# Kernel optimization log

Hardware: AMD Instinct MI355X
Metric: run time of the kernel (lower is better)

Reference implementation:

```python
import jax, jax.numpy as jnp
import numpy as np

EPS = 1e-6
HEADS = 8


def _block_weights(gh, gw):
    # block centers at (i+0.5, j+0.5); 'cos' transform, column-normalized (sum over dim 0)
    ii, jj = np.meshgrid(np.arange(gh) + 0.5, np.arange(gw) + 0.5, indexing='ij')
    centers = np.stack([ii.ravel(), jj.ravel()], axis=-1)  # [N, 2]
    d = np.linalg.norm(centers[:, None, :] - centers[None, :, :], axis=-1)  # [N, N]
    mat = np.cos(d / d.max() * np.pi / 4.0)
    mat = mat / mat.sum(axis=0, keepdims=True)
    return jnp.asarray(mat, dtype=jnp.float32)


def setup_inputs() -> dict:
    key = jax.random.key(0)
    ks = jax.random.split(key, 5)
    B, N, W, C = 8, 256, 49, 512
    s = 1.0 / np.sqrt(C)
    return {
        'x': jax.random.normal(ks[0], (B, N, W, C), jnp.float32),
        'ln_g': jnp.ones((C,), jnp.float32),
        'ln_b': jnp.zeros((C,), jnp.float32),
        'w_qkv': jax.random.normal(ks[1], (3 * C, C), jnp.float32) * s,  # Linear(dim, 3*dim, bias=False)
        'lepe_w': jax.random.normal(ks[2], (C, 1, 5, 5), jnp.float32) * 0.2,  # depthwise 5x5
        'lepe_b': jnp.zeros((C,), jnp.float32),
        'w_out': jax.random.normal(ks[3], (C, C), jnp.float32) * s,
        'b_out': jnp.zeros((C,), jnp.float32),
    }


def reference(x, ln_g, ln_b, w_qkv, lepe_w, lepe_b, w_out, b_out):
    B, N, Wn, C = x.shape
    H = HEADS
    D = C // H
    gh = gw = int(round(N ** 0.5))   # grid of window blocks
    wh = ww = int(round(Wn ** 0.5))  # tokens per window side

    # LayerNorm over channel dim (torch eps=1e-5, biased var)
    mu = x.mean(-1, keepdims=True)
    var = x.var(-1, keepdims=True)
    xn = (x - mu) / jnp.sqrt(var + 1e-5) * ln_g + ln_b

    # qkv projection
    qkv = jnp.einsum('bnwc,oc->bnwo', xn, w_qkv)
    q, k, v = jnp.split(qkv, 3, axis=-1)  # each [B, N, W, C]

    # LePE: fold v to image [B, C, gh*wh, gw*ww], depthwise conv 5x5 pad 2, unfold back
    img = v.reshape(B, gh, gw, wh, ww, C).transpose(0, 5, 1, 3, 2, 4).reshape(B, C, gh * wh, gw * ww)
    lepe = jax.lax.conv_general_dilated(
        img, lepe_w, window_strides=(1, 1), padding=((2, 2), (2, 2)),
        dimension_numbers=('NCHW', 'OIHW', 'NCHW'), feature_group_count=C)
    lepe = lepe + lepe_b[None, :, None, None]
    lepe = lepe.reshape(B, C, gh, wh, gw, ww).transpose(0, 2, 4, 3, 5, 1).reshape(B, N, Wn, C)

    # ReLU + eps feature maps (qk_norm=False -> identity norms)
    q = jax.nn.relu(q) + EPS
    k = jax.nn.relu(k) + EPS

    # split heads: [B, H, N, W, D]
    def split_heads(t):
        return t.reshape(B, N, Wn, H, D).transpose(0, 3, 1, 2, 4)
    q, k, v = split_heads(q), split_heads(k), split_heads(v)

    # per-block k^T v state: [B, H, N, D, D]
    kv = jnp.einsum('bhnwd,bhnwe->bhnde', k, v)
    weight = _block_weights(gh, gw)  # [N, N]
    kv = jnp.einsum('ij,bhjde->bhide', weight, kv)

    k_sum = k.sum(axis=-2)  # [B, H, N, D]
    qk_sum = jnp.einsum('bhnwd,bhnd->bhnw', q, k_sum)[..., None]  # [B, H, N, W, 1]
    normalizer = jnp.einsum('ij,bhjwo->bhiwo', weight, qk_sum) + EPS

    out = jnp.einsum('bhnwd,bhnde->bhnwe', q, kv) / normalizer  # [B, H, N, W, D]
    out = out.transpose(0, 2, 3, 1, 4).reshape(B, N, Wn, C)
    out = out + lepe
    return jnp.einsum('bnwc,oc->bnwo', out, w_out) + b_out
```

## Files before the change

### kernel.cpp

```cpp
#include <hip/hip_runtime.h>
#include <cstdint>

typedef unsigned short u16;
typedef unsigned int   u32;
typedef u16   u16x8 __attribute__((ext_vector_type(8)));
typedef u16   u16x4 __attribute__((ext_vector_type(4)));
typedef float f32x4 __attribute__((ext_vector_type(4)));
typedef __bf16 bf16x8 __attribute__((ext_vector_type(8)));

#define NB    256
#define WTOK  49
#define CH    512
#define HEADS 8
#define DH    64
#define TOK   100352
#define CO    1536

__device__ __forceinline__ u16 f2bf(float f) {
  u32 u = __float_as_uint(f);
  u = (u + 0x7FFFu + ((u >> 16) & 1u)) >> 16;
  return (u16)u;
}
__device__ __forceinline__ float bf2f(u16 u) { return __uint_as_float(((u32)u) << 16); }

__device__ __forceinline__ void load_lds16(const void* g, void* l) {
  __builtin_amdgcn_global_load_lds(
      reinterpret_cast<__attribute__((address_space(1))) void*>(reinterpret_cast<uintptr_t>(g)),
      reinterpret_cast<__attribute__((address_space(3))) void*>(reinterpret_cast<uintptr_t>(l)),
      16, 0, 0);
}

__global__ void cvt_f32_bf16(const float* __restrict__ in, u16* __restrict__ out, int n8) {
  int i = blockIdx.x * 256 + threadIdx.x;
  if (i < n8) {
    f32x4 a = *(const f32x4*)(in + (long)i * 8);
    f32x4 b = *(const f32x4*)(in + (long)i * 8 + 4);
    u16x8 o;
    o[0]=f2bf(a[0]); o[1]=f2bf(a[1]); o[2]=f2bf(a[2]); o[3]=f2bf(a[3]);
    o[4]=f2bf(b[0]); o[5]=f2bf(b[1]); o[6]=f2bf(b[2]); o[7]=f2bf(b[3]);
    *(u16x8*)(out + (long)i * 8) = o;
  }
}

__global__ void prep_wle(const float* __restrict__ lepe_w, float* __restrict__ wle) {
  int i = blockIdx.x * 256 + threadIdx.x;
  if (i < 12800) {
    int c = i / 25, kk = i % 25;
    wle[kk * 512 + c] = lepe_w[i];
  }
}

__global__ void weight_kernel(u16* __restrict__ Wbf, float* __restrict__ Wt) {
  int j = blockIdx.x, i = threadIdx.x;
  float iy = (float)(i >> 4) + 0.5f, ix = (float)(i & 15) + 0.5f;
  float jy = (float)(j >> 4) + 0.5f, jx = (float)(j & 15) + 0.5f;
  float dy = iy - jy, dx = ix - jx;
  float d = sqrtf(dy * dy + dx * dx);
  const float dmax = 21.213203435596427f;
  float m = cosf(d * (0.78539816339744831f / dmax));
  __shared__ float red[256];
  red[i] = m;
  __syncthreads();
  for (int s = 128; s > 0; s >>= 1) {
    if (i < s) red[i] += red[i + s];
    __syncthreads();
  }
  float w = m / red[0];
  Wbf[i * 256 + j] = f2bf(w);
  Wt[j * 256 + i] = w;
}

__global__ __launch_bounds__(256) void ln_kernel(const float* __restrict__ x,
                                                 const float* __restrict__ g,
                                                 const float* __restrict__ bta,
                                                 u16* __restrict__ xn) {
  int wave = threadIdx.x >> 6, lane = threadIdx.x & 63;
  long t = (long)blockIdx.x * 4 + wave;
  const float* xp = x + t * CH + lane * 8;
  f32x4 a = *(const f32x4*)xp;
  f32x4 b = *(const f32x4*)(xp + 4);
  float s  = a[0]+a[1]+a[2]+a[3]+b[0]+b[1]+b[2]+b[3];
  float sq = a[0]*a[0]+a[1]*a[1]+a[2]*a[2]+a[3]*a[3]+b[0]*b[0]+b[1]*b[1]+b[2]*b[2]+b[3]*b[3];
  for (int m = 1; m < 64; m <<= 1) { s += __shfl_xor(s, m); sq += __shfl_xor(sq, m); }
  float mu = s * (1.0f / 512.0f);
  float var = sq * (1.0f / 512.0f) - mu * mu;
  float rstd = rsqrtf(var + 1e-5f);
  const float* gp = g + lane * 8;
  const float* bp = bta + lane * 8;
  f32x4 g0 = *(const f32x4*)gp, g1 = *(const f32x4*)(gp + 4);
  f32x4 b0 = *(const f32x4*)bp, b1 = *(const f32x4*)(bp + 4);
  u16x8 o;
  o[0] = f2bf((a[0]-mu)*rstd*g0[0] + b0[0]);
  o[1] = f2bf((a[1]-mu)*rstd*g0[1] + b0[1]);
  o[2] = f2bf((a[2]-mu)*rstd*g0[2] + b0[2]);
  o[3] = f2bf((a[3]-mu)*rstd*g0[3] + b0[3]);
  o[4] = f2bf((b[0]-mu)*rstd*g1[0] + b1[0]);
  o[5] = f2bf((b[1]-mu)*rstd*g1[1] + b1[1]);
  o[6] = f2bf((b[2]-mu)*rstd*g1[2] + b1[2]);
  o[7] = f2bf((b[3]-mu)*rstd*g1[3] + b1[3]);
  *(u16x8*)(xn + t * CH + lane * 8) = o;
}

template <int KT>
__device__ __forceinline__ void kstep9(char* sm, const u16* sA, const u16* sB,
                                       int t, int lane_off, int wm, int wn,
                                       f32x4 (&acc)[8][4], bf16x8 (&fa)[2][8], bf16x8 (&fb)[2][4]) {
  constexpr int cur = KT & 1, nxt = cur ^ 1;
  if constexpr (KT + 4 < 16) {
    char* wbp = sm + ((KT + 4) & 3) * 32768 + t * 16;
    load_lds16(sA + (KT + 4) * 32, wbp);
    load_lds16(sA + (KT + 4) * 32 + 65536, wbp + 8192);
    load_lds16(sB + (KT + 4) * 32, wbp + 16384);
    load_lds16(sB + (KT + 4) * 32 + 65536, wbp + 24576);
  }
  if constexpr (KT + 1 < 16) {
    const char* base = sm + ((KT + 1) & 3) * 32768 + lane_off;
#pragma unroll
    for (int n = 0; n < 4; n++) fb[nxt][n] = *(const bf16x8*)(base + 16384 + wn * 4096 + n * 1024);
#pragma unroll
    for (int m = 0; m < 8; m++) fa[nxt][m] = *(const bf16x8*)(base + wm * 8192 + m * 1024);
  }
  __builtin_amdgcn_s_setprio(1);
#pragma unroll
  for (int m = 0; m < 8; m++)
#pragma unroll
    for (int n = 0; n < 4; n++)
      acc[m][n] = __builtin_amdgcn_mfma_f32_16x16x32_bf16(fa[cur][m], fb[cur][n], acc[m][n], 0, 0, 0);
  __builtin_amdgcn_s_setprio(0);
  if constexpr (KT < 14) {
    asm volatile("s_waitcnt lgkmcnt(0)" ::: "memory");
  }
  if constexpr (KT + 4 < 16) {
    asm volatile("s_waitcnt vmcnt(8)" ::: "memory");
  } else if constexpr (KT == 12) {
    asm volatile("s_waitcnt vmcnt(4)" ::: "memory");
  } else if constexpr (KT == 13) {
    asm volatile("s_waitcnt vmcnt(0)" ::: "memory");
  }
  if constexpr (KT < 14) __builtin_amdgcn_s_barrier();
}

template <int EPI>
__global__ __launch_bounds__(512, 2)
void gemm8(const u16* __restrict__ A, const u16* __restrict__ B,
           void* __restrict__ C, const float* __restrict__ bias, int N, int nbn) {
  __shared__ __align__(16) char sm[131072];
  const int nwg = gridDim.x;
  const int bid = blockIdx.x;
  const int cpx = nwg >> 3;
  const int vid = (bid & 7) * cpx + (bid >> 3);
  const int bn = vid % nbn, bm = vid / nbn;
  const int t = threadIdx.x;
  const int lane = t & 63, wave = t >> 6;
  const int wm = wave >> 2, wn = wave & 3;
  const int fr = lane & 15, fq = lane >> 4;
  const int lane_off = (fr >> 1) * 128 + ((((fr & 1) << 2) + fq) ^ (fr >> 1)) * 16;
  const int sl = (t & 7) ^ ((t >> 3) & 7);
  const u16* sA = A + ((long)bm * 256 + ((t >> 3) << 1) + (sl >> 2)) * 512 + (sl & 3) * 8;
  const u16* sB = B + ((long)bn * 256 + ((t >> 3) << 1) + (sl >> 2)) * 512 + (sl & 3) * 8;
  f32x4 acc[8][4] = {};
  bf16x8 fa[2][8], fb[2][4];
#pragma unroll
  for (int kt = 0; kt < 4; kt++) {
    char* d = sm + kt * 32768 + t * 16;
    load_lds16(sA + kt * 32, d);
    load_lds16(sA + kt * 32 + 65536, d + 8192);
    load_lds16(sB + kt * 32, d + 16384);
    load_lds16(sB + kt * 32 + 65536, d + 24576);
  }
  asm volatile("s_waitcnt vmcnt(8)" ::: "memory");
  __builtin_amdgcn_s_barrier();
  {
    const char* base = sm + lane_off;
#pragma unroll
    for (int n = 0; n < 4; n++) fb[0][n] = *(const bf16x8*)(base + 16384 + wn * 4096 + n * 1024);
#pragma unroll
    for (int m = 0; m < 8; m++) fa[0][m] = *(const bf16x8*)(base + wm * 8192 + m * 1024);
  }
  asm volatile("s_waitcnt lgkmcnt(0)" ::: "memory");
  __builtin_amdgcn_s_barrier();
  kstep9<0>(sm, sA, sB, t, lane_off, wm, wn, acc, fa, fb);
  kstep9<1>(sm, sA, sB, t, lane_off, wm, wn, acc, fa, fb);
  kstep9<2>(sm, sA, sB, t, lane_off, wm, wn, acc, fa, fb);
  kstep9<3>(sm, sA, sB, t, lane_off, wm, wn, acc, fa, fb);
  kstep9<4>(sm, sA, sB, t, lane_off, wm, wn, acc, fa, fb);
  kstep9<5>(sm, sA, sB, t, lane_off, wm, wn, acc, fa, fb);
  kstep9<6>(sm, sA, sB, t, lane_off, wm, wn, acc, fa, fb);
  kstep9<7>(sm, sA, sB, t, lane_off, wm, wn, acc, fa, fb);
  kstep9<8>(sm, sA, sB, t, lane_off, wm, wn, acc, fa, fb);
  kstep9<9>(sm, sA, sB, t, lane_off, wm, wn, acc, fa, fb);
  kstep9<10>(sm, sA, sB, t, lane_off, wm, wn, acc, fa, fb);
  kstep9<11>(sm, sA, sB, t, lane_off, wm, wn, acc, fa, fb);
  kstep9<12>(sm, sA, sB, t, lane_off, wm, wn, acc, fa, fb);
  kstep9<13>(sm, sA, sB, t, lane_off, wm, wn, acc, fa, fb);
  kstep9<14>(sm, sA, sB, t, lane_off, wm, wn, acc, fa, fb);
  kstep9<15>(sm, sA, sB, t, lane_off, wm, wn, acc, fa, fb);
  const long r0 = (long)bm * 256 + wm * 128 + fq * 4;
  const int c0 = bn * 256 + wn * 64 + fr;
#pragma unroll
  for (int m = 0; m < 8; m++) {
#pragma unroll
    for (int n = 0; n < 4; n++) {
      int c = c0 + n * 16;
#pragma unroll
      for (int jj = 0; jj < 4; jj++) {
        long r = r0 + m * 16 + jj;
        float v = acc[m][n][jj];
        if (EPI == 1) {
          if (c < 1024) v = fmaxf(v, 0.0f) + 1e-6f;
          ((u16*)C)[r * N + c] = f2bf(v);
        } else if (EPI == 2) {
          ((float*)C)[r * N + c] = v + bias[c];
        } else {
          ((u16*)C)[r * N + c] = f2bf(v);
        }
      }
    }
  }
}

template <int EPI>
__global__ __launch_bounds__(256)
void gemm_bt(const u16* __restrict__ A, const u16* __restrict__ B,
             void* __restrict__ C, const float* __restrict__ bias,
             int M, int N, int K, long sAb, long sBb, long sCb) {
  __shared__ u16 As[128 * 32];
  __shared__ u16 Bs[128 * 32];
  const int tid = threadIdx.x;
  const int lane = tid & 63;
  const int wave = tid >> 6;
  const int fr = lane & 15, fq = lane >> 4;
  const int wr = (wave >> 1) * 64, wc = (wave & 1) * 64;
  const long bm = blockIdx.y, bn = blockIdx.x, bz = blockIdx.z;
  const u16* Ab = A + bz * sAb + bm * 128 * (long)K;
  const u16* Bb = B + bz * sBb + bn * 128 * (long)K;
  const int srow = tid >> 2;
  const int scol = (tid & 3) * 8;
  f32x4 acc[4][4] = {};
  for (int k0 = 0; k0 < K; k0 += 32) {
    load_lds16(Ab + (long)srow * K + k0 + scol, As + tid * 8);
    load_lds16(Ab + (long)(srow + 64) * K + k0 + scol, As + 2048 + tid * 8);
    load_lds16(Bb + (long)srow * K + k0 + scol, Bs + tid * 8);
    load_lds16(Bb + (long)(srow + 64) * K + k0 + scol, Bs + 2048 + tid * 8);
    __syncthreads();
    bf16x8 af[4], bf[4];
#pragma unroll
    for (int m = 0; m < 4; m++) af[m] = *(const bf16x8*)&As[(wr + m * 16 + fr) * 32 + fq * 8];
#pragma unroll
    for (int n = 0; n < 4; n++) bf[n] = *(const bf16x8*)&Bs[(wc + n * 16 + fr) * 32 + fq * 8];
#pragma unroll
    for (int m = 0; m < 4; m++)
#pragma unroll
      for (int n = 0; n < 4; n++)
        acc[m][n] = __builtin_amdgcn_mfma_f32_16x16x32_bf16(af[m], bf[n], acc[m][n], 0, 0, 0);
    __syncthreads();
  }
#pragma unroll
  for (int m = 0; m < 4; m++) {
    int r0 = wr + m * 16 + fq * 4;
#pragma unroll
    for (int n = 0; n < 4; n++) {
      int c = (int)bn * 128 + wc + n * 16 + fr;
#pragma unroll
      for (int jj = 0; jj < 4; jj++) {
        long r = bm * 128 + r0 + jj;
        float v = acc[m][n][jj];
        if (EPI == 1) { if (c < 1024) v = fmaxf(v, 0.0f) + 1e-6f; }
        if (EPI == 2) {
          ((float*)C)[bz * sCb + r * N + c] = v + bias[c];
        } else {
          ((u16*)C)[bz * sCb + r * N + c] = f2bf(v);
        }
      }
    }
  }
}

__global__ __launch_bounds__(256)
void fold_v(const u16* __restrict__ qkv, u16* __restrict__ vimg) {
  long i = (long)blockIdx.x * 256 + threadIdx.x;
  int tok = (int)(i >> 6);
  int c0 = ((int)i & 63) * 8;
  int w = tok % WTOK, n = tok / WTOK;
  int b = n >> 8, blk = n & 255;
  int gi = blk >> 4, gj = blk & 15;
  int wi = w / 7, wj = w - wi * 7;
  int y = gi * 7 + wi + 2, x = gj * 7 + wj + 2;
  u16x8 v = *(const u16x8*)(qkv + (long)tok * CO + 1024 + c0);
  *(u16x8*)(vimg + (((long)(b * 116 + y)) * 116 + x) * 512 + c0) = v;
}

__global__ __launch_bounds__(256)
void zero_border(u16* __restrict__ vimg) {
  int y = blockIdx.x, b = blockIdx.y;
  int tid = threadIdx.x;
  u16* row = vimg + ((long)(b * 116 + y)) * 116 * 512;
  u16x8 z = {};
  if (y < 2 || y >= 114) {
    for (int i = tid; i < 116 * 512 / 8; i += 256) *(u16x8*)(row + i * 8) = z;
  } else {
    int col = tid >> 6;
    int x = (col < 2) ? col : 112 + col;
    *(u16x8*)(row + x * 512 + (tid & 63) * 8) = z;
  }
}

__global__ __launch_bounds__(256, 2)
void lepe_conv3(const u16* __restrict__ vimg, const float* __restrict__ wle,
                const float* __restrict__ lb, u16* __restrict__ lepe) {
  const int tid = threadIdx.x;
  const int c0 = (tid & 127) * 4;
  const int x  = blockIdx.x * 2 + (tid >> 7);
  const int ys = blockIdx.y * 14;
  const int b  = blockIdx.z;
  f32x4 wv[25];
#pragma unroll
  for (int k = 0; k < 25; k++) wv[k] = *(const f32x4*)(wle + k * 512 + c0);
  const f32x4 bias = *(const f32x4*)(lb + c0);
  const u16* rbase = vimg + (((long)(b * 116 + ys)) * 116 + x) * 512 + c0;
  u16x4 win[5][5];
#pragma unroll
  for (int j = 0; j < 4; j++) {
    const u16* rp = rbase + (long)j * (116 * 512);
#pragma unroll
    for (int kx = 0; kx < 5; kx++) win[j][kx] = *(const u16x4*)(rp + kx * 512);
  }
  const int gj = x / 7, wj = x - gj * 7;
  u16* ob = lepe + (((long)(b * 256 + blockIdx.y * 32 + gj)) * 49 + wj) * 512 + c0;
#pragma unroll
  for (int i = 0; i < 14; i++) {
    {
      const u16* rp = rbase + (long)(i + 4) * (116 * 512);
#pragma unroll
      for (int kx = 0; kx < 5; kx++) win[(i + 4) % 5][kx] = *(const u16x4*)(rp + kx * 512);
    }
    f32x4 acc = bias;
#pragma unroll
    for (int s = 0; s < 5; s++)
#pragma unroll
      for (int kx = 0; kx < 5; kx++) {
        u16x4 v = win[(i + s) % 5][kx];
        f32x4 w = wv[s * 5 + kx];
#pragma unroll
        for (int c = 0; c < 4; c++) acc[c] += bf2f(v[c]) * w[c];
      }
    u16x4 o;
#pragma unroll
    for (int c = 0; c < 4; c++) o[c] = f2bf(acc[c]);
    *(u16x4*)(ob + ((i / 7) * 784 + (i % 7) * 7) * 512) = o;
  }
}

__global__ __launch_bounds__(256)
void kv_local_kernel(const u16* __restrict__ qkv, u16* __restrict__ KVl,
                     float* __restrict__ qk_sum) {
  int n = blockIdx.x, h = blockIdx.y, b = blockIdx.z;
  int bh = b * HEADS + h;
  long tbase = ((long)(b * NB + n)) * WTOK;
  __shared__ u16 kT[64 * 72];
  __shared__ u16 vT[64 * 72];
  __shared__ u16 qs[49 * 72];
  __shared__ float ksum[64];
  __shared__ float qkp[256];
  int tid = threadIdx.x;
  for (int i = tid; i < (64 * 72) / 2; i += 256) {
    ((u32*)kT)[i] = 0;
    ((u32*)vT)[i] = 0;
  }
  __syncthreads();
  {
    int w = tid >> 3, d0 = (tid & 7) * 8;
    u16x8 k8 = *(const u16x8*)(qkv + (tbase + w) * CO + 512 + h * 64 + d0);
    u16x8 v8 = *(const u16x8*)(qkv + (tbase + w) * CO + 1024 + h * 64 + d0);
#pragma unroll
    for (int i = 0; i < 8; i++) { kT[(d0 + i) * 72 + w] = k8[i]; vT[(d0 + i) * 72 + w] = v8[i]; }
    int w2 = w + 32;
    if (w2 < WTOK) {
      u16x8 k82 = *(const u16x8*)(qkv + (tbase + w2) * CO + 512 + h * 64 + d0);
      u16x8 v82 = *(const u16x8*)(qkv + (tbase + w2) * CO + 1024 + h * 64 + d0);
#pragma unroll
      for (int i = 0; i < 8; i++) { kT[(d0 + i) * 72 + w2] = k82[i]; vT[(d0 + i) * 72 + w2] = v82[i]; }
    }
    if (tid < 196) {
      int wq = tid >> 2, dq = (tid & 3) * 16;
      u16x8 q0 = *(const u16x8*)(qkv + (tbase + wq) * CO + h * 64 + dq);
      u16x8 q1 = *(const u16x8*)(qkv + (tbase + wq) * CO + h * 64 + dq + 8);
      *(u16x8*)&qs[wq * 72 + dq] = q0;
      *(u16x8*)&qs[wq * 72 + dq + 8] = q1;
    }
  }
  __syncthreads();
  if (tid < 64) {
    float s = 0.0f;
#pragma unroll
    for (int c = 0; c < 9; c++) {
      u16x8 r = *(const u16x8*)&kT[tid * 72 + c * 8];
#pragma unroll
      for (int i = 0; i < 8; i++) s += bf2f(r[i]);
    }
    ksum[tid] = s;
  }
  __syncthreads();
  if (tid < 196) {
    int w = tid >> 2, d0 = (tid & 3) * 16;
    float s = 0.0f;
#pragma unroll
    for (int i = 0; i < 16; i++) s += bf2f(qs[w * 72 + d0 + i]) * ksum[d0 + i];
    qkp[tid] = s;
  }
  __syncthreads();
  if (tid < WTOK) {
    float s = qkp[tid * 4] + qkp[tid * 4 + 1] + qkp[tid * 4 + 2] + qkp[tid * 4 + 3];
    qk_sum[((long)bh * NB + n) * WTOK + tid] = s;
  }
  int lane = tid & 63, wave = tid >> 6;
  int fr = lane & 15, fq = lane >> 4;
  f32x4 acc[4] = {};
#pragma unroll
  for (int ks = 0; ks < 2; ks++) {
    bf16x8 a = *(const bf16x8*)&kT[(wave * 16 + fr) * 72 + ks * 32 + fq * 8];
#pragma unroll
    for (int n4 = 0; n4 < 4; n4++) {
      bf16x8 bb = *(const bf16x8*)&vT[(n4 * 16 + fr) * 72 + ks * 32 + fq * 8];
      acc[n4] = __builtin_amdgcn_mfma_f32_16x16x32_bf16(a, bb, acc[n4], 0, 0, 0);
    }
  }
  long obase = ((long)bh * NB + n) * 4096;
#pragma unroll
  for (int n4 = 0; n4 < 4; n4++)
#pragma unroll
    for (int jj = 0; jj < 4; jj++) {
      int d = wave * 16 + fq * 4 + jj;
      int e = n4 * 16 + fr;
      KVl[obase + d * 64 + e] = f2bf(acc[n4][jj]);
    }
}

__global__ __launch_bounds__(256)
void transpose_kv(const u16* __restrict__ in, u16* __restrict__ out) {
  int dt = blockIdx.x, jt = blockIdx.y, bh = blockIdx.z;
  __shared__ u16 t[64 * 72];
  int tid = threadIdx.x;
  {
    int jr = tid >> 2, c0 = (tid & 3) * 16;
    const u16* ip = in + ((long)bh * NB + jt * 64 + jr) * 4096 + dt * 64 + c0;
    *(u16x8*)&t[jr * 72 + c0] = *(const u16x8*)ip;
    *(u16x8*)&t[jr * 72 + c0 + 8] = *(const u16x8*)(ip + 8);
  }
  __syncthreads();
  {
    int der = tid >> 2, j0 = (tid & 3) * 16;
    u16x8 o0, o1;
#pragma unroll
    for (int i = 0; i < 8; i++) o0[i] = t[(j0 + i) * 72 + der];
#pragma unroll
    for (int i = 0; i < 8; i++) o1[i] = t[(j0 + 8 + i) * 72 + der];
    u16* op = out + ((long)bh * 4096 + dt * 64 + der) * 256 + jt * 64 + j0;
    *(u16x8*)op = o0;
    *(u16x8*)(op + 8) = o1;
  }
}

__global__ __launch_bounds__(256)
void norm_kernel(const float* __restrict__ Wt, const float* __restrict__ qk_sum,
                 float* __restrict__ inv_norm) {
  int bh = blockIdx.x, tid = threadIdx.x;
  __shared__ float qk[NB * WTOK];
  for (int i = tid; i < NB * WTOK; i += 256) qk[i] = qk_sum[(long)bh * NB * WTOK + i];
  __syncthreads();
  float acc[WTOK];
#pragma unroll
  for (int w = 0; w < WTOK; w++) acc[w] = 0.0f;
  for (int j = 0; j < NB; j++) {
    float wv = Wt[j * NB + tid];
#pragma unroll
    for (int w = 0; w < WTOK; w++) acc[w] += wv * qk[j * WTOK + w];
  }
  long ob = ((long)bh * NB + tid) * WTOK;
#pragma unroll
  for (int w = 0; w < WTOK; w++) inv_norm[ob + w] = 1.0f / (acc[w] + 1e-6f);
}

__global__ __launch_bounds__(256)
void attn_out_kernel(const u16* __restrict__ qkv, const u16* __restrict__ kvm,
                     const float* __restrict__ inv_norm, const u16* __restrict__ lepe,
                     u16* __restrict__ ebuf) {
  int n = blockIdx.x, h = blockIdx.y, b = blockIdx.z;
  int bh = b * HEADS + h;
  long tbase = ((long)(b * NB + n)) * WTOK;
  __shared__ u16 qs[64 * 72];
  __shared__ u16 kvT[64 * 72];
  __shared__ float inv[WTOK];
  int tid = threadIdx.x;
  if (tid < 196) {
    int w = tid >> 2, d0 = (tid & 3) * 16;
    u16x8 q0 = *(const u16x8*)(qkv + (tbase + w) * CO + h * 64 + d0);
    u16x8 q1 = *(const u16x8*)(qkv + (tbase + w) * CO + h * 64 + d0 + 8);
    *(u16x8*)&qs[w * 72 + d0] = q0;
    *(u16x8*)&qs[w * 72 + d0 + 8] = q1;
  }
  {
    int d = tid >> 2, e0 = (tid & 3) * 16;
    const u16* kp = kvm + ((long)bh * NB + n) * 4096 + d * 64 + e0;
    u16x8 k0 = *(const u16x8*)kp;
    u16x8 k1 = *(const u16x8*)(kp + 8);
#pragma unroll
    for (int i = 0; i < 8; i++) { kvT[(e0 + i) * 72 + d] = k0[i]; kvT[(e0 + 8 + i) * 72 + d] = k1[i]; }
  }
  if (tid < WTOK) inv[tid] = inv_norm[((long)bh * NB + n) * WTOK + tid];
  __syncthreads();
  int lane = tid & 63, wave = tid >> 6;
  int fr = lane & 15, fq = lane >> 4;
  f32x4 acc[4] = {};
#pragma unroll
  for (int ks = 0; ks < 2; ks++) {
    bf16x8 a = *(const bf16x8*)&qs[(wave * 16 + fr) * 72 + ks * 32 + fq * 8];
#pragma unroll
    for (int n4 = 0; n4 < 4; n4++) {
      bf16x8 bb = *(const bf16x8*)&kvT[(n4 * 16 + fr) * 72 + ks * 32 + fq * 8];
      acc[n4] = __builtin_amdgcn_mfma_f32_16x16x32_bf16(a, bb, acc[n4], 0, 0, 0);
    }
  }
#pragma unroll
  for (int n4 = 0; n4 < 4; n4++)
#pragma unroll
    for (int jj = 0; jj < 4; jj++) {
      int w = wave * 16 + fq * 4 + jj;
      if (w < WTOK) {
        int e = n4 * 16 + fr;
        long off = (tbase + w) * CH + h * 64 + e;
        float v = acc[n4][jj] * inv[w] + bf2f(lepe[off]);
        ebuf[off] = f2bf(v);
      }
    }
}

static const size_t OFF_XN    = 0;
static const size_t OFF_QKV   = 102760448;
static const size_t OFF_KVL   = OFF_QKV + 308281344;
static const size_t OFF_KVT   = OFF_KVL + 134217728;
static const size_t OFF_QKS   = OFF_KVT + 134217728;
static const size_t OFF_INV   = OFF_QKS + 3211264;
static const size_t OFF_WBF   = OFF_INV + 3211264;
static const size_t OFF_WTF   = OFF_WBF + 131072;
static const size_t OFF_WQKVB = OFF_WTF + 262144;
static const size_t OFF_WOUTB = OFF_WQKVB + 1572864;
static const size_t OFF_WLE   = OFF_WOUTB + 524288;

extern "C" void kernel_launch(void* const* d_in, const int* in_sizes, int n_in,
                              void* d_out, int out_size, void* d_ws, size_t ws_size,
                              hipStream_t stream) {
  const float* x      = (const float*)d_in[0];
  const float* ln_g   = (const float*)d_in[1];
  const float* ln_b   = (const float*)d_in[2];
  const float* w_qkv  = (const float*)d_in[3];
  const float* lepe_w = (const float*)d_in[4];
  const float* lepe_b = (const float*)d_in[5];
  const float* w_out  = (const float*)d_in[6];
  const float* b_out  = (const float*)d_in[7];
  float* out = (float*)d_out;
  char* ws = (char*)d_ws;

  u16*   xn     = (u16*)(ws + OFF_XN);
  u16*   lepe   = (u16*)(ws + OFF_XN);
  u16*   qkv    = (u16*)(ws + OFF_QKV);
  u16*   KVl    = (u16*)(ws + OFF_KVL);
  u16*   kvm    = (u16*)(ws + OFF_KVL);
  u16*   vimg   = (u16*)(ws + OFF_KVT);
  u16*   KVT    = (u16*)(ws + OFF_KVT);
  u16*   ebuf   = (u16*)(ws + OFF_KVT);
  float* qks    = (float*)(ws + OFF_QKS);
  float* invn   = (float*)(ws + OFF_INV);
  u16*   Wbf    = (u16*)(ws + OFF_WBF);
  float* Wt     = (float*)(ws + OFF_WTF);
  u16*   wqkvb  = (u16*)(ws + OFF_WQKVB);
  u16*   woutb  = (u16*)(ws + OFF_WOUTB);
  float* wle    = (float*)(ws + OFF_WLE);

  cvt_f32_bf16<<<384, 256, 0, stream>>>(w_qkv, wqkvb, 98304);
  cvt_f32_bf16<<<128, 256, 0, stream>>>(w_out, woutb, 32768);
  prep_wle<<<50, 256, 0, stream>>>(lepe_w, wle);
  weight_kernel<<<256, 256, 0, stream>>>(Wbf, Wt);
  zero_border<<<dim3(116, 8), 256, 0, stream>>>(vimg);

  ln_kernel<<<25088, 256, 0, stream>>>(x, ln_g, ln_b, xn);

  gemm8<1><<<2352, 512, 0, stream>>>(xn, wqkvb, (void*)qkv, nullptr, CO, 6);

  fold_v<<<25088, 256, 0, stream>>>(qkv, vimg);
  lepe_conv3<<<dim3(56, 8, 8), 256, 0, stream>>>(vimg, wle, lepe_b, lepe);

  kv_local_kernel<<<dim3(NB, HEADS, 8), 256, 0, stream>>>(qkv, KVl, qks);

  transpose_kv<<<dim3(64, 4, 64), 256, 0, stream>>>(KVl, KVT);

  gemm_bt<0><<<dim3(32, 2, 64), 256, 0, stream>>>(Wbf, KVT, (void*)kvm, nullptr,
                                                  NB, 4096, NB,
                                                  0, (long)4096 * 256, (long)256 * 4096);

  norm_kernel<<<64, 256, 0, stream>>>(Wt, qks, invn);

  attn_out_kernel<<<dim3(NB, HEADS, 8), 256, 0, stream>>>(qkv, kvm, invn, lepe, ebuf);

  gemm8<2><<<784, 512, 0, stream>>>(ebuf, woutb, (void*)out, b_out, CH, 2);
}
```

Measured before the change: 906.8 us.

## Load A fragments directly from global and stage B in two LDS halves

Result: slower. 1.151 ms (+27.0%).

```diff
diff --git a/kernel.cpp b/kernel.cpp
--- a/kernel.cpp
+++ b/kernel.cpp
@@ -101,100 +101,86 @@
   *(u16x8*)(xn + t * CH + lane * 8) = o;
 }
 
-template <int KT>
-__device__ __forceinline__ void kstep9(char* sm, const u16* sA, const u16* sB,
-                                       int t, int lane_off, int wm, int wn,
-                                       f32x4 (&acc)[8][4], bf16x8 (&fa)[2][8], bf16x8 (&fb)[2][4]) {
-  constexpr int cur = KT & 1, nxt = cur ^ 1;
-  if constexpr (KT + 4 < 16) {
-    char* wbp = sm + ((KT + 4) & 3) * 32768 + t * 16;
-    load_lds16(sA + (KT + 4) * 32, wbp);
-    load_lds16(sA + (KT + 4) * 32 + 65536, wbp + 8192);
-    load_lds16(sB + (KT + 4) * 32, wbp + 16384);
-    load_lds16(sB + (KT + 4) * 32 + 65536, wbp + 24576);
-  }
-  if constexpr (KT + 1 < 16) {
-    const char* base = sm + ((KT + 1) & 3) * 32768 + lane_off;
-#pragma unroll
-    for (int n = 0; n < 4; n++) fb[nxt][n] = *(const bf16x8*)(base + 16384 + wn * 4096 + n * 1024);
-#pragma unroll
-    for (int m = 0; m < 8; m++) fa[nxt][m] = *(const bf16x8*)(base + wm * 8192 + m * 1024);
-  }
-  __builtin_amdgcn_s_setprio(1);
-#pragma unroll
-  for (int m = 0; m < 8; m++)
-#pragma unroll
-    for (int n = 0; n < 4; n++)
-      acc[m][n] = __builtin_amdgcn_mfma_f32_16x16x32_bf16(fa[cur][m], fb[cur][n], acc[m][n], 0, 0, 0);
-  __builtin_amdgcn_s_setprio(0);
-  if constexpr (KT < 14) {
-    asm volatile("s_waitcnt lgkmcnt(0)" ::: "memory");
-  }
-  if constexpr (KT + 4 < 16) {
-    asm volatile("s_waitcnt vmcnt(8)" ::: "memory");
-  } else if constexpr (KT == 12) {
-    asm volatile("s_waitcnt vmcnt(4)" ::: "memory");
-  } else if constexpr (KT == 13) {
-    asm volatile("s_waitcnt vmcnt(0)" ::: "memory");
-  }
-  if constexpr (KT < 14) __builtin_amdgcn_s_barrier();
-}
-
 template <int EPI>
 __global__ __launch_bounds__(512, 2)
-void gemm8(const u16* __restrict__ A, const u16* __restrict__ B,
+void gemmA(const u16* __restrict__ A, const u16* __restrict__ B,
            void* __restrict__ C, const float* __restrict__ bias, int N, int nbn) {
-  __shared__ __align__(16) char sm[131072];
-  const int nwg = gridDim.x;
-  const int bid = blockIdx.x;
+  __shared__ __align__(16) u16 Bs[256 * 256];
+  const int nwg = gridDim.x, bid = blockIdx.x;
   const int cpx = nwg >> 3;
   const int vid = (bid & 7) * cpx + (bid >> 3);
   const int bn = vid % nbn, bm = vid / nbn;
-  const int t = threadIdx.x;
-  const int lane = t & 63, wave = t >> 6;
+  const int t = threadIdx.x, lane = t & 63, wave = t >> 6;
   const int wm = wave >> 2, wn = wave & 3;
   const int fr = lane & 15, fq = lane >> 4;
-  const int lane_off = (fr >> 1) * 128 + ((((fr & 1) << 2) + fq) ^ (fr >> 1)) * 16;
-  const int sl = (t & 7) ^ ((t >> 3) & 7);
-  const u16* sA = A + ((long)bm * 256 + ((t >> 3) << 1) + (sl >> 2)) * 512 + (sl & 3) * 8;
-  const u16* sB = B + ((long)bn * 256 + ((t >> 3) << 1) + (sl >> 2)) * 512 + (sl & 3) * 8;
+
+  const u16* pA[8];
+#pragma unroll
+  for (int m = 0; m < 8; m++)
+    pA[m] = A + ((long)(bm * 256 + wm * 128 + m * 16 + fr)) * 512 + fq * 8;
+
+  const u16* sBp = B + ((long)(bn * 256 + (t >> 5))) * 512
+                   + (((t & 31) ^ ((t >> 5) & 7)) * 8);
+
+  const int bxor = (fr & 7) * 16;
+  int brb[4];
+#pragma unroll
+  for (int n = 0; n < 4; n++) brb[n] = (wn * 64 + n * 16 + fr) * 512;
+
   f32x4 acc[8][4] = {};
-  bf16x8 fa[2][8], fb[2][4];
-#pragma unroll
-  for (int kt = 0; kt < 4; kt++) {
-    char* d = sm + kt * 32768 + t * 16;
-    load_lds16(sA + kt * 32, d);
-    load_lds16(sA + kt * 32 + 65536, d + 8192);
-    load_lds16(sB + kt * 32, d + 16384);
-    load_lds16(sB + kt * 32 + 65536, d + 24576);
-  }
-  asm volatile("s_waitcnt vmcnt(8)" ::: "memory");
-  __builtin_amdgcn_s_barrier();
-  {
-    const char* base = sm + lane_off;
-#pragma unroll
-    for (int n = 0; n < 4; n++) fb[0][n] = *(const bf16x8*)(base + 16384 + wn * 4096 + n * 1024);
-#pragma unroll
-    for (int m = 0; m < 8; m++) fa[0][m] = *(const bf16x8*)(base + wm * 8192 + m * 1024);
-  }
-  asm volatile("s_waitcnt lgkmcnt(0)" ::: "memory");
-  __builtin_amdgcn_s_barrier();
-  kstep9<0>(sm, sA, sB, t, lane_off, wm, wn, acc, fa, fb);
-  kstep9<1>(sm, sA, sB, t, lane_off, wm, wn, acc, fa, fb);
-  kstep9<2>(sm, sA, sB, t, lane_off, wm, wn, acc, fa, fb);
-  kstep9<3>(sm, sA, sB, t, lane_off, wm, wn, acc, fa, fb);
-  kstep9<4>(sm, sA, sB, t, lane_off, wm, wn, acc, fa, fb);
-  kstep9<5>(sm, sA, sB, t, lane_off, wm, wn, acc, fa, fb);
-  kstep9<6>(sm, sA, sB, t, lane_off, wm, wn, acc, fa, fb);
-  kstep9<7>(sm, sA, sB, t, lane_off, wm, wn, acc, fa, fb);
-  kstep9<8>(sm, sA, sB, t, lane_off, wm, wn, acc, fa, fb);
-  kstep9<9>(sm, sA, sB, t, lane_off, wm, wn, acc, fa, fb);
-  kstep9<10>(sm, sA, sB, t, lane_off, wm, wn, acc, fa, fb);
-  kstep9<11>(sm, sA, sB, t, lane_off, wm, wn, acc, fa, fb);
-  kstep9<12>(sm, sA, sB, t, lane_off, wm, wn, acc, fa, fb);
-  kstep9<13>(sm, sA, sB, t, lane_off, wm, wn, acc, fa, fb);
-  kstep9<14>(sm, sA, sB, t, lane_off, wm, wn, acc, fa, fb);
-  kstep9<15>(sm, sA, sB, t, lane_off, wm, wn, acc, fa, fb);
+  bf16x8 fa0[8], fa1[8];
+
+#define STAGE_B(K0)                                                          \
+  _Pragma("unroll") for (int rd = 0; rd < 16; rd++)                          \
+      load_lds16(sBp + (K0) + rd * 8192, (char*)Bs + rd * 8192 + t * 16);
+
+#define STEP(KQ, FCUR, FNXT, KNXT, DOPREF)                                   \
+  {                                                                          \
+    if (DOPREF) {                                                            \
+      _Pragma("unroll") for (int m = 0; m < 8; m++)                          \
+          FNXT[m] = *(const bf16x8*)(pA[m] + (KNXT));                        \
+    }                                                                        \
+    bf16x8 fb[4];                                                            \
+    _Pragma("unroll") for (int n = 0; n < 4; n++) {                          \
+      int off = brb[n] + ((((KQ) * 4 + fq) * 16) ^ bxor);                    \
+      fb[n] = *(const bf16x8*)((const char*)Bs + off);                       \
+    }                                                                        \
+    _Pragma("unroll") for (int m = 0; m < 8; m++)                            \
+      _Pragma("unroll") for (int n = 0; n < 4; n++)                          \
+        acc[m][n] = __builtin_amdgcn_mfma_f32_16x16x32_bf16(                 \
+            FCUR[m], fb[n], acc[m][n], 0, 0, 0);                             \
+  }
+
+  STAGE_B(0);
+#pragma unroll
+  for (int m = 0; m < 8; m++) fa0[m] = *(const bf16x8*)(pA[m]);
+  __syncthreads();
+
+  STEP(0, fa0, fa1, 32, true)
+  STEP(1, fa1, fa0, 64, true)
+  STEP(2, fa0, fa1, 96, true)
+  STEP(3, fa1, fa0, 128, true)
+  STEP(4, fa0, fa1, 160, true)
+  STEP(5, fa1, fa0, 192, true)
+  STEP(6, fa0, fa1, 224, true)
+  STEP(7, fa1, fa0, 256, true)
+
+  __syncthreads();
+  STAGE_B(256);
+  __syncthreads();
+
+  STEP(0, fa0, fa1, 288, true)
+  STEP(1, fa1, fa0, 320, true)
+  STEP(2, fa0, fa1, 352, true)
+  STEP(3, fa1, fa0, 384, true)
+  STEP(4, fa0, fa1, 416, true)
+  STEP(5, fa1, fa0, 448, true)
+  STEP(6, fa0, fa1, 480, true)
+  STEP(7, fa1, fa0, 0, false)
+
+#undef STAGE_B
+#undef STEP
+
   const long r0 = (long)bm * 256 + wm * 128 + fq * 4;
   const int c0 = bn * 256 + wn * 64 + fr;
 #pragma unroll
@@ -585,7 +571,7 @@
 
   ln_kernel<<<25088, 256, 0, stream>>>(x, ln_g, ln_b, xn);
 
-  gemm8<1><<<2352, 512, 0, stream>>>(xn, wqkvb, (void*)qkv, nullptr, CO, 6);
+  gemmA<1><<<2352, 512, 0, stream>>>(xn, wqkvb, (void*)qkv, nullptr, CO, 6);
 
   fold_v<<<25088, 256, 0, stream>>>(qkv, vimg);
   lepe_conv3<<<dim3(56, 8, 8), 256, 0, stream>>>(vimg, wle, lepe_b, lepe);
@@ -602,5 +588,5 @@
 
   attn_out_kernel<<<dim3(NB, HEADS, 8), 256, 0, stream>>>(qkv, kvm, invn, lepe, ebuf);
 
-  gemm8<2><<<784, 512, 0, stream>>>(ebuf, woutb, (void*)out, b_out, CH, 2);
-}
+  gemmA<2><<<784, 512, 0, stream>>>(ebuf, woutb, (void*)out, b_out, CH, 2);
+}
```
